# Kernel tuning notes

Hardware: AMD Instinct MI355X
Metric: run time of the kernel (lower is better)

The kernel has to match this reference:

```python
import jax, jax.numpy as jnp
import numpy as np

# Constants from UpFIRDn2dJIT(channel=64, lrelu_upsampling=2, filter_size=6, kernel_size=3)
# with init_kernel(in_size=128, out_size=128): up_factor = dn_factor = 2.
UP = 2
DN = 2
SLOPE = 0.2
GAIN = 1.4142135623730951  # sqrt(2)
CROP = 1  # kernel_size - 1 - kernel_size//2 for kernel_size=3
IN_SIZE = 128
FILTER_SIZE = 6
B, C = 8, 64


def _firwin_lowpass(numtaps, cutoff, width, fs):
    # Reproduces scipy.signal.firwin(numtaps, cutoff, width=width, fs=fs)
    # (lowpass, pass_zero=True, scale=True, Kaiser window from `width`).
    nyq = 0.5 * fs
    atten = 2.285 * (numtaps - 1) * np.pi * (width / nyq) + 7.95  # kaiser_atten
    if atten > 50:
        beta = 0.1102 * (atten - 8.7)
    elif atten > 21:
        beta = 0.5842 * (atten - 21) ** 0.4 + 0.07886 * (atten - 21)
    else:
        beta = 0.0
    m = np.arange(numtaps) - (numtaps - 1) / 2.0
    c = cutoff / nyq
    h = c * np.sinc(c * m) * np.kaiser(numtaps, beta)
    h = h / h.sum()  # scale so DC gain == 1
    return h.astype(np.float32)


def _conv1d_same(x, f, axis):
    # x: [N, 1, H, W]; 1D cross-correlation along `axis` (2 or 3) with torch
    # padding='same' semantics for even taps: left pad = (K-1)//2, right pad gets the extra.
    K = f.shape[0]
    pl = (K - 1) // 2
    pr = (K - 1) - pl
    if axis == 2:
        kern = f.reshape(1, 1, K, 1)
        pad = [(pl, pr), (0, 0)]
    else:
        kern = f.reshape(1, 1, 1, K)
        pad = [(0, 0), (pl, pr)]
    return jax.lax.conv_general_dilated(
        x, kern, window_strides=(1, 1), padding=pad,
        dimension_numbers=("NCHW", "OIHW", "NCHW"))


def _forward(x, bias, up_filter, dn_filter):
    x = x[:, :, CROP:-CROP, CROP:-CROP]            # [B, C, 128, 128]
    b, c, h, w = x.shape
    x = x + bias[None, :, None, None]
    x = x.reshape(b * c, 1, h, w)
    x = jnp.repeat(jnp.repeat(x, UP, axis=2), UP, axis=3)
    # outer(f, f) conv == separable 1D convs (filter is an outer product)
    x = _conv1d_same(_conv1d_same(x, up_filter, 2), up_filter, 3)
    x = jnp.where(x >= 0, x, SLOPE * x) * GAIN     # leaky ReLU * gain
    x = _conv1d_same(_conv1d_same(x, dn_filter, 2), dn_filter, 3)
    x = x[:, :, ::DN, ::DN]                        # grid_pool2d -> [B*C, 1, 128, 128]
    return x.reshape(b, c, x.shape[2], x.shape[3])


def setup_inputs() -> dict:
    key = jax.random.key(0)
    kx, = jax.random.split(key, 1)
    x = jax.random.normal(kx, (B, C, IN_SIZE + 2 * CROP, IN_SIZE + 2 * CROP), dtype=jnp.float32)
    bias = jnp.zeros((C,), dtype=jnp.float32)  # nn.Parameter init to zeros
    taps = FILTER_SIZE * UP  # 12
    up_filter = jnp.asarray(_firwin_lowpass(taps, IN_SIZE / 2.0001, IN_SIZE, IN_SIZE))
    dn_filter = jnp.asarray(_firwin_lowpass(taps, IN_SIZE / 2.0001, IN_SIZE, IN_SIZE))
    return {"x": x, "bias": bias, "up_filter": up_filter, "dn_filter": dn_filter}


def reference(x, bias, up_filter, dn_filter):
    return _forward(x, bias, up_filter, dn_filter)
```

## Files before the change

kernel.cpp:

```cpp
#include <hip/hip_runtime.h>


#define GAIN_C 1.4142135623730951f
#define NEG_C ((0.2f - 1.0f) * GAIN_C)

typedef short v8s __attribute__((ext_vector_type(8)));
typedef float v4f __attribute__((ext_vector_type(4)));

__device__ __forceinline__ int f2bf(float f) {
    unsigned u = __float_as_uint(f);
    return (int)((u + 0x7FFFu + ((u >> 16) & 1u)) >> 16) & 0xFFFF;
}
__device__ __forceinline__ int pack_bf2(float a, float b) {
#if __has_builtin(__builtin_amdgcn_cvt_pk_bf16_f32)
    typedef __bf16 bf2 __attribute__((ext_vector_type(2)));
    bf2 r = __builtin_amdgcn_cvt_pk_bf16_f32(a, b);
    int o; __builtin_memcpy(&o, &r, 4); return o;
#else
    return f2bf(a) | (f2bf(b) << 16);
#endif
}

__device__ float band(int x, int q, const float* fu) {
    if (q >= 74 || x >= 43 || x < 0) return 0.f;
    int p = q >> 1, d = x - p;
    if (q & 1) {
        if (d < 0 || d > 6) return 0.f;
        if (d == 0) return fu[0];
        if (d == 6) return fu[11];
        return fu[2 * d - 1] + fu[2 * d];
    } else {
        if (d < 0 || d > 5) return 0.f;
        return fu[2 * d] + fu[2 * d + 1];
    }
}
__device__ float dband(int o, int q, int v, const float* fd) {
    if (q >= 74 || q < 0) return 0.f;
    if (v == 0 && q < 5) return 0.f;
    if (v == 2 && q >= 69) return 0.f;
    int k = q - 2 * o;
    if (k < 0 || k > 11) return 0.f;
    return fd[k];
}

__global__ __launch_bounds__(256) void build_consts(
    const float* __restrict__ fu, const float* __restrict__ fd,
    short* __restrict__ ws)
{
    int idx = blockIdx.x * 256 + threadIdx.x;
    int l = (idx >> 3) & 63, j = idx & 7;
    int l15 = l & 15, kq = (l >> 4) * 8 + j;
    float val;
    if (idx < 2560) {
        int nt = idx >> 9;
        int k0 = 8 * nt < 16 ? 8 * nt : 16;
        val = band(k0 + kq, 16 * nt + l15, fu);
    } else if (idx < 5120) {
        int mt = (idx - 2560) >> 9;
        int k0 = 8 * mt < 16 ? 8 * mt : 16;
        val = band(k0 + kq, 16 * mt + l15, fu);
    } else if (idx < 11264) {
        int rel = idx - 5120;
        int v = rel >> 11, fi = (rel & 2047) >> 9;
        int mt = fi >> 1, kt = fi & 1;
        int pp = (mt ? 16 : 0) + 32 * kt + kq;
        val = dband(16 * mt + l15, pp, v, fd);
    } else {
        int rel = idx - 11264;
        int v = rel >> 11, fi = (rel & 2047) >> 9;
        int nt = fi >> 1, kt = fi & 1;
        int qq = (nt ? 16 : 0) + 32 * kt + kq;
        val = dband(16 * nt + l15, qq, v, fd);
    }
    ws[idx] = (short)f2bf(val);
}

#define XPITCH 48
#define BPITCH 48
#define UPITCH 88
#define TPITCH 80

__global__ __launch_bounds__(320, 8) void upfirdn_mfma(
    const float* __restrict__ xin_all,
    const float* __restrict__ bias,
    const short* __restrict__ cws,
    float* __restrict__ out)
{
    __shared__ __align__(16) short SH[2304 + 3840 + 7040];
    short* Xl  = SH;
    short* B1t = SH + 2304;
    short* Ut  = SH + 6144;
    short* T   = SH;

    const int tid  = threadIdx.x;
    const int lane = tid & 63, w = tid >> 6;
    const int l15  = lane & 15, q4 = lane >> 4;
    const int bx = blockIdx.x, by = blockIdx.y, bc = blockIdx.z;
    const int i0 = by * 32, j0 = bx * 32;

    const short* GtB = cws;
    const short* G2A = cws + 2560;
    const short* DA  = cws + 5120  + ((by == 0) ? 0 : (by == 3) ? 2 : 1) * 2048;
    const short* D2B = cws + 11264 + ((bx == 0) ? 0 : (bx == 3) ? 2 : 1) * 2048;

    {
        const float* xp = xin_all + (size_t)bc * (130 * 130);
        const float bv = bias[bc & 63];
        const bool colInt = (bx == 1) | (bx == 2);
        int* Xli = (int*)Xl;
        for (int idx = tid; idx < 1152; idx += 320) {
            int r = idx / 24, cp = idx - r * 24;
            int gr = i0 - 5 + r;
            float f0 = 0.f, f1 = 0.f;
            if (r < 43 && (unsigned)gr < 128u && cp < 22) {
                const float* rowp = xp + (gr + 1) * 130 + 1;
                int gc0 = j0 - 5 + 2 * cp;
                if (colInt) {
                    f0 = rowp[gc0] + bv;
                    if (cp < 21) f1 = rowp[gc0 + 1] + bv;
                } else {
                    if ((unsigned)gc0 < 128u) f0 = rowp[gc0] + bv;
                    if (cp < 21 && (unsigned)(gc0 + 1) < 128u)
                        f1 = rowp[gc0 + 1] + bv;
                }
            }
            Xli[r * 24 + cp] = pack_bf2(f0, f1);
        }
    }
    __syncthreads();

    {
        const int nt = w;
        const int k0 = 8 * nt < 16 ? 8 * nt : 16;
        v8s bf = *(const v8s*)&GtB[nt * 512 + lane * 8];
#pragma unroll
        for (int mt = 0; mt < 3; ++mt) {
            v8s a = *(const v8s*)&Xl[(16 * mt + l15) * XPITCH + k0 + q4 * 8];
            v4f acc = {0.f, 0.f, 0.f, 0.f};
            acc = __builtin_amdgcn_mfma_f32_16x16x32_bf16(a, bf, acc, 0, 0, 0);
            *(int2*)&B1t[(16 * nt + l15) * BPITCH + 16 * mt + q4 * 4] =
                make_int2(pack_bf2(acc[0], acc[1]), pack_bf2(acc[2], acc[3]));
        }
    }
    __syncthreads();

    {
        const int mt = w;
        const int k0 = 8 * mt < 16 ? 8 * mt : 16;
        v8s af = *(const v8s*)&G2A[mt * 512 + lane * 8];
#pragma unroll
        for (int nt = 0; nt < 5; ++nt) {
            v8s b = *(const v8s*)&B1t[(16 * nt + l15) * BPITCH + k0 + q4 * 8];
            v4f acc = {0.f, 0.f, 0.f, 0.f};
            acc = __builtin_amdgcn_mfma_f32_16x16x32_bf16(af, b, acc, 0, 0, 0);
#pragma unroll
            for (int i = 0; i < 4; ++i)
                acc[i] = GAIN_C * acc[i] + NEG_C * fminf(acc[i], 0.f);
            *(int2*)&Ut[(16 * nt + l15) * UPITCH + 16 * mt + q4 * 4] =
                make_int2(pack_bf2(acc[0], acc[1]), pack_bf2(acc[2], acc[3]));
        }
    }
    __syncthreads();

    {
        const int nt = w;
#pragma unroll
        for (int mt = 0; mt < 2; ++mt) {
            const int k0 = mt ? 16 : 0;
            v4f acc = {0.f, 0.f, 0.f, 0.f};
#pragma unroll
            for (int kt = 0; kt < 2; ++kt) {
                v8s a = *(const v8s*)&DA[(mt * 2 + kt) * 512 + lane * 8];
                v8s b = *(const v8s*)&Ut[(16 * nt + l15) * UPITCH
                                         + k0 + 32 * kt + q4 * 8];
                acc = __builtin_amdgcn_mfma_f32_16x16x32_bf16(a, b, acc, 0, 0, 0);
            }
#pragma unroll
            for (int i = 0; i < 4; ++i)
                T[(16 * mt + q4 * 4 + i) * TPITCH + 16 * nt + l15] =
                    (short)f2bf(acc[i]);
        }
    }
    __syncthreads();

    if (w < 4) {
        const int mt = w >> 1, nt = w & 1;
        const int k0 = nt ? 16 : 0;
        v4f acc = {0.f, 0.f, 0.f, 0.f};
#pragma unroll
        for (int kt = 0; kt < 2; ++kt) {
            v8s a = *(const v8s*)&T[(16 * mt + l15) * TPITCH + k0 + 32 * kt + q4 * 8];
            v8s b = *(const v8s*)&D2B[(nt * 2 + kt) * 512 + lane * 8];
            acc = __builtin_amdgcn_mfma_f32_16x16x32_bf16(a, b, acc, 0, 0, 0);
        }
        float* op = out + (size_t)bc * 16384
                  + (size_t)(i0 + 16 * mt + q4 * 4) * 128 + (j0 + 16 * nt + l15);
#pragma unroll
        for (int i = 0; i < 4; ++i) op[i * 128] = acc[i];
    }
}

extern "C" void kernel_launch(void* const* d_in, const int* in_sizes, int n_in,
                              void* d_out, int out_size, void* d_ws, size_t ws_size,
                              hipStream_t stream) {
    const float* x  = (const float*)d_in[0];
    const float* bs = (const float*)d_in[1];
    const float* fu = (const float*)d_in[2];
    const float* fd = (const float*)d_in[3];
    float* outp = (float*)d_out;
    short* ws = (short*)d_ws;

    build_consts<<<68, 256, 0, stream>>>(fu, fd, ws);
    upfirdn_mfma<<<dim3(4, 4, 512), 320, 0, stream>>>(x, bs, ws, outp);
}
```

Before: 123.2 us.

## Enlarge output tile to 64x32 rows to cut halo recomputation

Each block now computes a 64-row by 32-column output tile with 512 threads instead of 32x32 with 320 threads, which halves the grid in the row direction. The larger tile reduces the fraction of halo rows loaded and recomputed through the upsample, activation and downsample matrix stages. The constant banded filter matrices are rebuilt for the taller tile, and the boundary variants in the row direction drop from three to two. Shared memory per block rises and the work loops use strided wave assignment, which may leave some waves idle and can lower occupancy.

```diff
diff --git a/kernel.cpp b/kernel.cpp
--- a/kernel.cpp
+++ b/kernel.cpp
@@ -21,8 +21,8 @@
 #endif
 }
 
-__device__ float band(int x, int q, const float* fu) {
-    if (q >= 74 || x >= 43 || x < 0) return 0.f;
+__device__ float band(int x, int q, int qlim, int xlim, const float* fu) {
+    if (q >= qlim || x >= xlim || x < 0) return 0.f;
     int p = q >> 1, d = x - p;
     if (q & 1) {
         if (d < 0 || d > 6) return 0.f;
@@ -34,10 +34,10 @@
         return fu[2 * d] + fu[2 * d + 1];
     }
 }
-__device__ float dband(int o, int q, int v, const float* fd) {
-    if (q >= 74 || q < 0) return 0.f;
+__device__ float dband(int o, int q, int v, int qlim, const float* fd) {
+    if (q >= qlim || q < 0) return 0.f;
     if (v == 0 && q < 5) return 0.f;
-    if (v == 2 && q >= 69) return 0.f;
+    if (v == 2 && q >= qlim - 5) return 0.f;
     int k = q - 2 * o;
     if (k < 0 || k > 11) return 0.f;
     return fd[k];
@@ -54,65 +54,66 @@
     if (idx < 2560) {
         int nt = idx >> 9;
         int k0 = 8 * nt < 16 ? 8 * nt : 16;
-        val = band(k0 + kq, 16 * nt + l15, fu);
-    } else if (idx < 5120) {
+        val = band(k0 + kq, 16 * nt + l15, 74, 43, fu);
+    } else if (idx < 7168) {
         int mt = (idx - 2560) >> 9;
-        int k0 = 8 * mt < 16 ? 8 * mt : 16;
-        val = band(k0 + kq, 16 * mt + l15, fu);
-    } else if (idx < 11264) {
-        int rel = idx - 5120;
-        int v = rel >> 11, fi = (rel & 2047) >> 9;
+        int k0 = 8 * mt < 48 ? 8 * mt : 48;
+        val = band(k0 + kq, 16 * mt + l15, 138, 75, fu);
+    } else if (idx < 15360) {
+        int rel = idx - 7168;
+        int v = (rel >> 12) ? 2 : 0;
+        int fi = (rel & 4095) >> 9;
         int mt = fi >> 1, kt = fi & 1;
-        int pp = (mt ? 16 : 0) + 32 * kt + kq;
-        val = dband(16 * mt + l15, pp, v, fd);
+        int k0 = 32 * mt < 80 ? 32 * mt : 80;
+        val = dband(16 * mt + l15, k0 + 32 * kt + kq, v, 138, fd);
     } else {
-        int rel = idx - 11264;
+        int rel = idx - 15360;
         int v = rel >> 11, fi = (rel & 2047) >> 9;
         int nt = fi >> 1, kt = fi & 1;
-        int qq = (nt ? 16 : 0) + 32 * kt + kq;
-        val = dband(16 * nt + l15, qq, v, fd);
+        int k0 = nt ? 16 : 0;
+        val = dband(16 * nt + l15, k0 + 32 * kt + kq, v, 74, fd);
     }
     ws[idx] = (short)f2bf(val);
 }
 
 #define XPITCH 48
-#define BPITCH 48
-#define UPITCH 88
-#define TPITCH 80
-
-__global__ __launch_bounds__(320, 8) void upfirdn_mfma(
+#define BPITCH 88
+#define UPITCH 152
+#define TPITCH 88
+
+__global__ __launch_bounds__(512, 8) void upfirdn_mfma(
     const float* __restrict__ xin_all,
     const float* __restrict__ bias,
     const short* __restrict__ cws,
     float* __restrict__ out)
 {
-    __shared__ __align__(16) short SH[2304 + 3840 + 7040];
-    short* Xl  = SH;
-    short* B1t = SH + 2304;
-    short* Ut  = SH + 6144;
+    __shared__ __align__(16) short SH[19200];
+    short* B1t = SH;
+    short* Ut  = SH + 7040;
+    short* Xl  = SH + 7040;
     short* T   = SH;
 
     const int tid  = threadIdx.x;
     const int lane = tid & 63, w = tid >> 6;
     const int l15  = lane & 15, q4 = lane >> 4;
     const int bx = blockIdx.x, by = blockIdx.y, bc = blockIdx.z;
-    const int i0 = by * 32, j0 = bx * 32;
+    const int i0 = by * 64, j0 = bx * 32;
 
     const short* GtB = cws;
     const short* G2A = cws + 2560;
-    const short* DA  = cws + 5120  + ((by == 0) ? 0 : (by == 3) ? 2 : 1) * 2048;
-    const short* D2B = cws + 11264 + ((bx == 0) ? 0 : (bx == 3) ? 2 : 1) * 2048;
+    const short* DA  = cws + 7168  + (by ? 4096 : 0);
+    const short* D2B = cws + 15360 + ((bx == 0) ? 0 : (bx == 3) ? 2 : 1) * 2048;
 
     {
         const float* xp = xin_all + (size_t)bc * (130 * 130);
         const float bv = bias[bc & 63];
         const bool colInt = (bx == 1) | (bx == 2);
         int* Xli = (int*)Xl;
-        for (int idx = tid; idx < 1152; idx += 320) {
+        for (int idx = tid; idx < 1920; idx += 512) {
             int r = idx / 24, cp = idx - r * 24;
             int gr = i0 - 5 + r;
             float f0 = 0.f, f1 = 0.f;
-            if (r < 43 && (unsigned)gr < 128u && cp < 22) {
+            if (r < 75 && (unsigned)gr < 128u && cp < 22) {
                 const float* rowp = xp + (gr + 1) * 130 + 1;
                 int gc0 = j0 - 5 + 2 * cp;
                 if (colInt) {
@@ -129,61 +130,52 @@
     }
     __syncthreads();
 
-    {
-        const int nt = w;
+    for (int t = w; t < 25; t += 8) {
+        const int mt = t / 5, nt = t - mt * 5;
         const int k0 = 8 * nt < 16 ? 8 * nt : 16;
         v8s bf = *(const v8s*)&GtB[nt * 512 + lane * 8];
-#pragma unroll
-        for (int mt = 0; mt < 3; ++mt) {
-            v8s a = *(const v8s*)&Xl[(16 * mt + l15) * XPITCH + k0 + q4 * 8];
-            v4f acc = {0.f, 0.f, 0.f, 0.f};
-            acc = __builtin_amdgcn_mfma_f32_16x16x32_bf16(a, bf, acc, 0, 0, 0);
-            *(int2*)&B1t[(16 * nt + l15) * BPITCH + 16 * mt + q4 * 4] =
-                make_int2(pack_bf2(acc[0], acc[1]), pack_bf2(acc[2], acc[3]));
+        v8s a  = *(const v8s*)&Xl[(16 * mt + l15) * XPITCH + k0 + q4 * 8];
+        v4f acc = {0.f, 0.f, 0.f, 0.f};
+        acc = __builtin_amdgcn_mfma_f32_16x16x32_bf16(a, bf, acc, 0, 0, 0);
+        *(int2*)&B1t[(16 * nt + l15) * BPITCH + 16 * mt + q4 * 4] =
+            make_int2(pack_bf2(acc[0], acc[1]), pack_bf2(acc[2], acc[3]));
+    }
+    __syncthreads();
+
+    for (int t = w; t < 45; t += 8) {
+        const int mt = t / 5, nt = t - mt * 5;
+        const int k0 = 8 * mt < 48 ? 8 * mt : 48;
+        v8s af = *(const v8s*)&G2A[mt * 512 + lane * 8];
+        v8s b  = *(const v8s*)&B1t[(16 * nt + l15) * BPITCH + k0 + q4 * 8];
+        v4f acc = {0.f, 0.f, 0.f, 0.f};
+        acc = __builtin_amdgcn_mfma_f32_16x16x32_bf16(af, b, acc, 0, 0, 0);
+#pragma unroll
+        for (int i = 0; i < 4; ++i)
+            acc[i] = GAIN_C * acc[i] + NEG_C * fminf(acc[i], 0.f);
+        *(int2*)&Ut[(16 * nt + l15) * UPITCH + 16 * mt + q4 * 4] =
+            make_int2(pack_bf2(acc[0], acc[1]), pack_bf2(acc[2], acc[3]));
+    }
+    __syncthreads();
+
+    for (int t = w; t < 20; t += 8) {
+        const int mt = t / 5, nt = t - mt * 5;
+        const int k0 = 32 * mt < 80 ? 32 * mt : 80;
+        v4f acc = {0.f, 0.f, 0.f, 0.f};
+#pragma unroll
+        for (int kt = 0; kt < 2; ++kt) {
+            v8s a = *(const v8s*)&DA[(mt * 2 + kt) * 512 + lane * 8];
+            v8s b = *(const v8s*)&Ut[(16 * nt + l15) * UPITCH
+                                     + k0 + 32 * kt + q4 * 8];
+            acc = __builtin_amdgcn_mfma_f32_16x16x32_bf16(a, b, acc, 0, 0, 0);
         }
+#pragma unroll
+        for (int i = 0; i < 4; ++i)
+            T[(16 * mt + q4 * 4 + i) * TPITCH + 16 * nt + l15] =
+                (short)f2bf(acc[i]);
     }
     __syncthreads();
 
     {
-        const int mt = w;
-        const int k0 = 8 * mt < 16 ? 8 * mt : 16;
-        v8s af = *(const v8s*)&G2A[mt * 512 + lane * 8];
-#pragma unroll
-        for (int nt = 0; nt < 5; ++nt) {
-            v8s b = *(const v8s*)&B1t[(16 * nt + l15) * BPITCH + k0 + q4 * 8];
-            v4f acc = {0.f, 0.f, 0.f, 0.f};
-            acc = __builtin_amdgcn_mfma_f32_16x16x32_bf16(af, b, acc, 0, 0, 0);
-#pragma unroll
-            for (int i = 0; i < 4; ++i)
-                acc[i] = GAIN_C * acc[i] + NEG_C * fminf(acc[i], 0.f);
-            *(int2*)&Ut[(16 * nt + l15) * UPITCH + 16 * mt + q4 * 4] =
-                make_int2(pack_bf2(acc[0], acc[1]), pack_bf2(acc[2], acc[3]));
-        }
-    }
-    __syncthreads();
-
-    {
-        const int nt = w;
-#pragma unroll
-        for (int mt = 0; mt < 2; ++mt) {
-            const int k0 = mt ? 16 : 0;
-            v4f acc = {0.f, 0.f, 0.f, 0.f};
-#pragma unroll
-            for (int kt = 0; kt < 2; ++kt) {
-                v8s a = *(const v8s*)&DA[(mt * 2 + kt) * 512 + lane * 8];
-                v8s b = *(const v8s*)&Ut[(16 * nt + l15) * UPITCH
-                                         + k0 + 32 * kt + q4 * 8];
-                acc = __builtin_amdgcn_mfma_f32_16x16x32_bf16(a, b, acc, 0, 0, 0);
-            }
-#pragma unroll
-            for (int i = 0; i < 4; ++i)
-                T[(16 * mt + q4 * 4 + i) * TPITCH + 16 * nt + l15] =
-                    (short)f2bf(acc[i]);
-        }
-    }
-    __syncthreads();
-
-    if (w < 4) {
         const int mt = w >> 1, nt = w & 1;
         const int k0 = nt ? 16 : 0;
         v4f acc = {0.f, 0.f, 0.f, 0.f};
@@ -210,6 +202,6 @@
     float* outp = (float*)d_out;
     short* ws = (short*)d_ws;
 
-    build_consts<<<68, 256, 0, stream>>>(fu, fd, ws);
-    upfirdn_mfma<<<dim3(4, 4, 512), 320, 0, stream>>>(x, bs, ws, outp);
-}
+    build_consts<<<84, 256, 0, stream>>>(fu, fd, ws);
+    upfirdn_mfma<<<dim3(4, 2, 512), 512, 0, stream>>>(x, bs, ws, outp);
+}
```

Measured after the change: 120.6 us. -2.1%, faster.
